# Kernel optimization log

Hardware: AMD Instinct MI355X
Metric: run time of the kernel (lower is better)

## Reference

```python
import jax, jax.numpy as jnp
import numpy as np

EPS = 1e-6

def fexp(x, p):
    # signed power used in superquadric parametrization
    return jnp.sign(x) * (jnp.abs(x) + EPS) ** p

def quat_to_rot(q):
    q = q / (jnp.linalg.norm(q, axis=-1, keepdims=True) + EPS)
    w, x, y, z = q[..., 0], q[..., 1], q[..., 2], q[..., 3]
    R = jnp.stack([
        jnp.stack([1 - 2 * (y * y + z * z), 2 * (x * y - w * z), 2 * (x * z + w * y)], -1),
        jnp.stack([2 * (x * y + w * z), 1 - 2 * (x * x + z * z), 2 * (y * z - w * x)], -1),
        jnp.stack([2 * (x * z - w * y), 2 * (y * z + w * x), 1 - 2 * (x * x + y * y)], -1),
    ], -2)
    return R  # (..., 3, 3)

def setup_inputs() -> dict:
    key = jax.random.key(0)
    ks = jax.random.split(key, 9)
    B, M, S, N = 8, 16, 100, 2048
    pcl = jax.random.normal(ks[0], (B, N, 3), jnp.float32)
    translations = 0.5 * jax.random.normal(ks[1], (B, M, 3), jnp.float32)
    rotations = jax.random.normal(ks[2], (B, M, 4), jnp.float32)
    size = 0.2 + 0.6 * jax.random.uniform(ks[3], (B, M, 3), jnp.float32)
    shape_eps = 0.4 + 1.2 * jax.random.uniform(ks[4], (B, M, 2), jnp.float32)
    deformations = 0.6 * jax.random.uniform(ks[5], (B, M, 2), jnp.float32) - 0.3
    probabilities = jax.random.uniform(ks[6], (B, M), jnp.float32, 0.05, 0.95)
    etas = jax.random.uniform(ks[7], (S,), jnp.float32, -np.pi / 2, np.pi / 2)
    omegas = jax.random.uniform(ks[8], (S,), jnp.float32, -np.pi, np.pi)
    return {"pcl": pcl, "translations": translations, "rotations": rotations,
            "size": size, "shape_eps": shape_eps, "deformations": deformations,
            "probabilities": probabilities, "etas": etas, "omegas": omegas}

def reference(pcl, translations, rotations, size, shape_eps, deformations, probabilities, etas, omegas):
    B, N, _ = pcl.shape
    M = translations.shape[1]
    # transform pcl into primitive-centric frames: (B,N,M,3)
    R = quat_to_rot(rotations)                                   # (B,M,3,3)
    d = pcl[:, :, None, :] - translations[:, None, :, :]         # (B,N,M,3)
    pcl_t = jnp.einsum('bmij,bnmj->bnmi', R, d)                  # (B,N,M,3)
    # sample superquadric surfaces: (B,M,S,3)
    e1 = shape_eps[..., 0:1]; e2 = shape_eps[..., 1:2]           # (B,M,1)
    a1 = size[..., 0:1]; a2 = size[..., 1:2]; a3 = size[..., 2:3]
    ce = fexp(jnp.cos(etas)[None, None, :], e1)
    se = fexp(jnp.sin(etas)[None, None, :], e1)
    cw = fexp(jnp.cos(omegas)[None, None, :], e2)
    sw = fexp(jnp.sin(omegas)[None, None, :], e2)
    x = a1 * ce * cw; y = a2 * ce * sw; z = a3 * se              # (B,M,S)
    # tapering deformation
    fx = deformations[..., 0:1] * z / a3 + 1.0
    fy = deformations[..., 1:2] * z / a3 + 1.0
    points = jnp.stack([fx * x, fy * y, z], -1)                  # (B,M,S,3)
    # pairwise squared distances: (B,M,S,N)
    diff = points[:, :, :, None, :] - jnp.transpose(pcl_t, (0, 2, 1, 3))[:, :, None, :, :]
    dist = jnp.sum(diff * diff, -1)
    # --- pcl_to_prim loss ---
    dmin = jnp.transpose(jnp.min(dist, axis=2), (0, 2, 1))       # (B,N,M)
    idx = jnp.argsort(dmin, axis=-1)
    distance = jnp.take_along_axis(dmin, idx, axis=-1)
    probs_g = jax.vmap(lambda p, i: p[i])(probabilities, idx)    # (B,N,M)
    neg_cp = jnp.cumprod(1.0 - probs_g, axis=-1)
    neg_cp = jnp.concatenate([jnp.ones_like(neg_cp[..., :1]), neg_cp[..., :-1]], -1)
    minprob = probs_g * neg_cp
    pcl_to_prim = jnp.sum(distance * minprob) / (B * N)
    # --- prim_to_pcl loss ---
    dminN = jnp.min(dist, axis=3)                                # (B,M,S)
    dminN = jnp.where(dminN >= 1e30, 0.0, dminN)
    s0, s1, s2 = size[..., 0], size[..., 1], size[..., 2]
    area = 4 * np.pi * ((s0 * s1) ** 1.6 / 3 + (s0 * s2) ** 1.6 / 3 + (s1 * s2) ** 1.6 / 3) ** 0.625
    area = M * area / jnp.sum(area, axis=-1, keepdims=True)
    prim_to_pcl = jnp.sum(jnp.mean(dminN, -1) * area) / (B * M)
    # regularizer weights are zero (regularizer_type=None path) -> regs = 0
    return pcl_to_prim + prim_to_pcl
```

## Files before the change

### kernel.cpp

```cpp
#include <hip/hip_runtime.h>
#include <math.h>

#define EPSF 1e-6f

constexpr int B = 8, N = 2048, M = 16, S = 100;
constexpr int MAIN_BLOCKS = B * (N / 64);
constexpr int PRIM_BLOCKS = B * M * 2;
constexpr int TOTAL_BLOCKS = MAIN_BLOCKS + PRIM_BLOCKS;
constexpr int NPART = MAIN_BLOCKS * 4 + PRIM_BLOCKS;

typedef float v2f __attribute__((ext_vector_type(2)));

__device__ __forceinline__ float hw_exp2(float x) { return __builtin_amdgcn_exp2f(x); }
__device__ __forceinline__ float hw_log2(float x) { return __builtin_amdgcn_logf(x); }

__device__ __forceinline__ float fexp_d(float x, float p) {
    float sg = (x > 0.f) ? 1.f : ((x < 0.f) ? -1.f : 0.f);
    return sg * __powf(fabsf(x) + EPSF, p);
}

__device__ __forceinline__ float sgn_d(float x) {
    return (x > 0.f) ? 1.f : ((x < 0.f) ? -1.f : 0.f);
}

__device__ __forceinline__ void quat_Rv(float w, float x, float y, float z, float R[9]) {
    float inv = 1.0f / (sqrtf(w * w + x * x + y * y + z * z) + EPSF);
    w *= inv; x *= inv; y *= inv; z *= inv;
    R[0] = 1.f - 2.f * (y * y + z * z); R[1] = 2.f * (x * y - w * z); R[2] = 2.f * (x * z + w * y);
    R[3] = 2.f * (x * y + w * z); R[4] = 1.f - 2.f * (x * x + z * z); R[5] = 2.f * (y * z - w * x);
    R[6] = 2.f * (x * z - w * y); R[7] = 2.f * (y * z + w * x); R[8] = 1.f - 2.f * (x * x + y * y);
}

__device__ __forceinline__ void quat_R(const float* __restrict__ rot, int bm, float R[9]) {
    quat_Rv(rot[bm * 4 + 0], rot[bm * 4 + 1], rot[bm * 4 + 2], rot[bm * 4 + 3], R);
}

__device__ __forceinline__ float4 surf_point(
    const float* __restrict__ sizep, const float* __restrict__ seps,
    const float* __restrict__ deform, const float* __restrict__ etas,
    const float* __restrict__ omegas, int bm, int s)
{
    float e1 = seps[bm * 2 + 0], e2 = seps[bm * 2 + 1];
    float a1 = sizep[bm * 3 + 0], a2 = sizep[bm * 3 + 1], a3 = sizep[bm * 3 + 2];
    float d0 = deform[bm * 2 + 0], d1 = deform[bm * 2 + 1];
    float se_, ce_, sw_, cw_;
    __sincosf(etas[s], &se_, &ce_);
    __sincosf(omegas[s], &sw_, &cw_);
    float ce = fexp_d(ce_, e1);
    float se = fexp_d(se_, e1);
    float cw = fexp_d(cw_, e2);
    float sw = fexp_d(sw_, e2);
    float x = a1 * ce * cw;
    float y = a2 * ce * sw;
    float z = a3 * se;
    float fx = d0 * (z / a3) + 1.0f;
    float fy = d1 * (z / a3) + 1.0f;
    float4 P;
    P.x = fx * x; P.y = fy * y; P.z = z;
    P.w = P.x * P.x + P.y * P.y + P.z * P.z;
    return P;
}

__global__ __launch_bounds__(256) void k_all(
    const float* __restrict__ pcl, const float* __restrict__ trans,
    const float* __restrict__ rot, const float* __restrict__ sizep,
    const float* __restrict__ seps, const float* __restrict__ deform,
    const float* __restrict__ probs,
    const float* __restrict__ etas, const float* __restrict__ omegas,
    float* __restrict__ part, unsigned int* __restrict__ flags,
    float* __restrict__ out)
{
    __shared__ float4 pts[S * M];
    __shared__ __align__(16) float trig[S * 8];
    __shared__ float sbuf[20];

    int t = threadIdx.x;

    if (blockIdx.x < MAIN_BLOCKS) {
        int b  = blockIdx.x >> 5;
        int n0 = (blockIdx.x & 31) * 64;
        int m  = t & 15;
        int nl = t >> 4;
        int bm = b * M + m;

        float qw = rot[bm * 4 + 0], qx = rot[bm * 4 + 1];
        float qy = rot[bm * 4 + 2], qz = rot[bm * 4 + 3];
        float tx = trans[bm * 3 + 0], ty = trans[bm * 3 + 1], tz = trans[bm * 3 + 2];
        float plx[4], ply[4], plz[4];
#pragma unroll
        for (int j = 0; j < 4; j++) {
            int n = n0 + nl + 16 * j;
            plx[j] = pcl[(b * N + n) * 3 + 0];
            ply[j] = pcl[(b * N + n) * 3 + 1];
            plz[j] = pcl[(b * N + n) * 3 + 2];
        }
        float pv = probs[bm];

        float4* trig4 = (float4*)trig;
        if (t < S) {
            float se_, ce_, sw_, cw_;
            __sincosf(etas[t], &se_, &ce_);
            __sincosf(omegas[t], &sw_, &cw_);
            float4 tA, tB;
            tA.x = hw_log2(fabsf(ce_) + EPSF); tA.y = sgn_d(ce_);
            tA.z = hw_log2(fabsf(se_) + EPSF); tA.w = sgn_d(se_);
            tB.x = hw_log2(fabsf(cw_) + EPSF); tB.y = sgn_d(cw_);
            tB.z = hw_log2(fabsf(sw_) + EPSF); tB.w = sgn_d(sw_);
            trig4[t * 2 + 0] = tA;
            trig4[t * 2 + 1] = tB;
        }
        __syncthreads();

        {
            float e1 = seps[bm * 2 + 0], e2 = seps[bm * 2 + 1];
            float a1 = sizep[bm * 3 + 0], a2 = sizep[bm * 3 + 1], a3 = sizep[bm * 3 + 2];
            float d0 = deform[bm * 2 + 0], d1 = deform[bm * 2 + 1];
            for (int s = nl; s < S; s += 16) {
                float4 tA = trig4[s * 2 + 0];
                float4 tB = trig4[s * 2 + 1];
                float ce = tA.y * hw_exp2(e1 * tA.x);
                float se = tA.w * hw_exp2(e1 * tA.z);
                float cw = tB.y * hw_exp2(e2 * tB.x);
                float sw = tB.w * hw_exp2(e2 * tB.z);
                float x = a1 * ce * cw;
                float y = a2 * ce * sw;
                float z = a3 * se;
                float fx = fmaf(d0, se, 1.0f);
                float fy = fmaf(d1, se, 1.0f);
                float4 P;
                P.x = fx * x; P.y = fy * y; P.z = z;
                P.w = P.x * P.x + P.y * P.y + P.z * P.z;
                pts[s * M + m] = P;
            }
        }
        __syncthreads();

        float R[9];
        quat_Rv(qw, qx, qy, qz, R);

        v2f mx2[2], my2[2], mz2[2], dmin2[2];
        float psq[4];
#pragma unroll
        for (int j = 0; j < 4; j++) {
            float dx = plx[j] - tx, dy = ply[j] - ty, dz = plz[j] - tz;
            float X = R[0] * dx + R[1] * dy + R[2] * dz;
            float Y = R[3] * dx + R[4] * dy + R[5] * dz;
            float Z = R[6] * dx + R[7] * dy + R[8] * dz;
            mx2[j >> 1][j & 1] = -2.f * X;
            my2[j >> 1][j & 1] = -2.f * Y;
            mz2[j >> 1][j & 1] = -2.f * Z;
            psq[j] = X * X + Y * Y + Z * Z;
            dmin2[j >> 1][j & 1] = 3.4e38f;
        }

        auto compute4 = [&](const float4* P4) {
#pragma unroll
            for (int u = 0; u < 4; u++) {
                float4 P = P4[u];
                v2f vx = {P.x, P.x}, vy = {P.y, P.y}, vz = {P.z, P.z}, vw = {P.w, P.w};
#pragma unroll
                for (int p = 0; p < 2; p++) {
                    v2f d = __builtin_elementwise_fma(vx, mx2[p], vw);
                    d = __builtin_elementwise_fma(vy, my2[p], d);
                    d = __builtin_elementwise_fma(vz, mz2[p], d);
                    dmin2[p] = __builtin_elementwise_min(dmin2[p], d);
                }
            }
        };
        auto load8 = [&](float4* dst, int sbase) {
#pragma unroll
            for (int u = 0; u < 8; u++) dst[u] = pts[(sbase + u) * M + m];
        };

        float4 Abank[8], Bbank[8];
        load8(Abank, 0);
        for (int gp = 0; gp < 6; gp++) {
            load8(Bbank, (2 * gp + 1) * 8);
            compute4(Abank); compute4(Abank + 4);
            if (gp < 5) load8(Abank, (2 * gp + 2) * 8);
            else {
#pragma unroll
                for (int u = 0; u < 4; u++) Abank[u] = pts[(96 + u) * M + m];
            }
            compute4(Bbank); compute4(Bbank + 4);
        }
        compute4(Abank);

        float ompr[16];
#pragma unroll
        for (int k = 0; k < 16; k++) ompr[k] = 1.f - probs[b * M + k];
        float acc = 0.f;
#pragma unroll
        for (int j = 0; j < 4; j++) {
            float key = dmin2[j >> 1][j & 1] + psq[j];
            float prod = 1.f;
#pragma unroll
            for (int k = 0; k < 16; k++) {
                float bk = __shfl(key, k, 16);
                bool before = (bk < key) || (bk == key && k < m);
                prod *= before ? ompr[k] : 1.f;
            }
            acc += key * pv * prod;
        }
        for (int off = 32; off >= 1; off >>= 1) acc += __shfl_down(acc, off);
        if ((t & 63) == 0)
            __hip_atomic_store(&part[blockIdx.x * 4 + (t >> 6)],
                               acc * (1.0f / (B * N)),
                               __ATOMIC_RELAXED, __HIP_MEMORY_SCOPE_AGENT);
        __syncthreads();
        if (t == 0)
            __hip_atomic_store(&flags[blockIdx.x], 1u,
                               __ATOMIC_RELEASE, __HIP_MEMORY_SCOPE_AGENT);
    } else {
        int pb = blockIdx.x - MAIN_BLOCKS;
        int bm = pb >> 1, q = pb & 1;
        int b = bm >> 4, m = bm & 15;
        int s0 = q * 50;

        float4* spts = pts;
        float* sarea = sbuf;
        float* wsum  = sbuf + 16;

        if (t < 50) spts[t] = surf_point(sizep, seps, deform, etas, omegas, bm, s0 + t);
        if (t >= 64 && t < 64 + M) {
            int mm = t - 64;
            float s0s = sizep[(b * M + mm) * 3 + 0];
            float s1s = sizep[(b * M + mm) * 3 + 1];
            float s2s = sizep[(b * M + mm) * 3 + 2];
            float tt = __powf(s0s * s1s, 1.6f) / 3.f + __powf(s0s * s2s, 1.6f) / 3.f
                     + __powf(s1s * s2s, 1.6f) / 3.f;
            sarea[mm] = 4.0f * 3.14159265358979323846f * __powf(tt, 0.625f);
        }
        __syncthreads();

        float R[9];
        quat_R(rot, bm, R);
        float tx = trans[bm * 3 + 0], ty = trans[bm * 3 + 1], tz = trans[bm * 3 + 2];

        int w = t >> 6, lane = t & 63;
        int cnt = (w < 2) ? 13 : 12;
        int off = (w < 2) ? w * 13 : 26 + (w - 2) * 12;

        v2f px2[7], py2[7], pz2[7], mins2[7];
#pragma unroll
        for (int k = 0; k < 14; k++) {
            int sl = (k < cnt) ? (off + k) : off;
            float4 P = spts[sl];
            px2[k >> 1][k & 1] = P.x;
            py2[k >> 1][k & 1] = P.y;
            pz2[k >> 1][k & 1] = P.z;
            mins2[k >> 1][k & 1] = 3.4e38f;
        }

        const float* pcb = pcl + b * N * 3 + lane * 3;

#define LOADG(x0,y0,z0,x1,y1,z1,x2,y2,z2,x3,y3,z3, g)            \
        { const float* p_ = pcb + (g) * 768;                     \
          x0 = p_[0];   y0 = p_[1];   z0 = p_[2];                \
          x1 = p_[192]; y1 = p_[193]; z1 = p_[194];              \
          x2 = p_[384]; y2 = p_[385]; z2 = p_[386];              \
          x3 = p_[576]; y3 = p_[577]; z3 = p_[578]; }

#define COMP1(cx,cy,cz)                                          \
        { float dx = (cx) - tx, dy = (cy) - ty, dz = (cz) - tz;  \
          float X = R[0] * dx + R[1] * dy + R[2] * dz;           \
          float Y = R[3] * dx + R[4] * dy + R[5] * dz;           \
          float Z = R[6] * dx + R[7] * dy + R[8] * dz;           \
          float Xsq = X * X + Y * Y + Z * Z;                     \
          v2f vmX = {-2.f * X, -2.f * X}, vmY = {-2.f * Y, -2.f * Y}; \
          v2f vmZ = {-2.f * Z, -2.f * Z}, vXq = {Xsq, Xsq};      \
          _Pragma("unroll")                                      \
          for (int k = 0; k < 7; k++) {                          \
              v2f d = __builtin_elementwise_fma(px2[k], vmX, vXq); \
              d = __builtin_elementwise_fma(py2[k], vmY, d);     \
              d = __builtin_elementwise_fma(pz2[k], vmZ, d);     \
              mins2[k] = __builtin_elementwise_min(mins2[k], d); \
          } }

#define COMPG(x0,y0,z0,x1,y1,z1,x2,y2,z2,x3,y3,z3)               \
        COMP1(x0,y0,z0) COMP1(x1,y1,z1) COMP1(x2,y2,z2) COMP1(x3,y3,z3)

        float a0x,a0y,a0z,a1x,a1y,a1z,a2x,a2y,a2z,a3x,a3y,a3z;
        float b0x,b0y,b0z,b1x,b1y,b1z,b2x,b2y,b2z,b3x,b3y,b3z;

        LOADG(a0x,a0y,a0z,a1x,a1y,a1z,a2x,a2y,a2z,a3x,a3y,a3z, 0)
        LOADG(b0x,b0y,b0z,b1x,b1y,b1z,b2x,b2y,b2z,b3x,b3y,b3z, 1)
        COMPG(a0x,a0y,a0z,a1x,a1y,a1z,a2x,a2y,a2z,a3x,a3y,a3z)
        LOADG(a0x,a0y,a0z,a1x,a1y,a1z,a2x,a2y,a2z,a3x,a3y,a3z, 2)
        COMPG(b0x,b0y,b0z,b1x,b1y,b1z,b2x,b2y,b2z,b3x,b3y,b3z)
        LOADG(b0x,b0y,b0z,b1x,b1y,b1z,b2x,b2y,b2z,b3x,b3y,b3z, 3)
        COMPG(a0x,a0y,a0z,a1x,a1y,a1z,a2x,a2y,a2z,a3x,a3y,a3z)
        LOADG(a0x,a0y,a0z,a1x,a1y,a1z,a2x,a2y,a2z,a3x,a3y,a3z, 4)
        COMPG(b0x,b0y,b0z,b1x,b1y,b1z,b2x,b2y,b2z,b3x,b3y,b3z)
        LOADG(b0x,b0y,b0z,b1x,b1y,b1z,b2x,b2y,b2z,b3x,b3y,b3z, 5)
        COMPG(a0x,a0y,a0z,a1x,a1y,a1z,a2x,a2y,a2z,a3x,a3y,a3z)
        LOADG(a0x,a0y,a0z,a1x,a1y,a1z,a2x,a2y,a2z,a3x,a3y,a3z, 6)
        COMPG(b0x,b0y,b0z,b1x,b1y,b1z,b2x,b2y,b2z,b3x,b3y,b3z)
        LOADG(b0x,b0y,b0z,b1x,b1y,b1z,b2x,b2y,b2z,b3x,b3y,b3z, 7)
        COMPG(a0x,a0y,a0z,a1x,a1y,a1z,a2x,a2y,a2z,a3x,a3y,a3z)
        COMPG(b0x,b0y,b0z,b1x,b1y,b1z,b2x,b2y,b2z,b3x,b3y,b3z)

#undef LOADG
#undef COMP1
#undef COMPG

        float sum = 0.f;
#pragma unroll
        for (int k = 0; k < 14; k++) {
            float v = mins2[k >> 1][k & 1];
            for (int o = 32; o >= 1; o >>= 1) v = fminf(v, __shfl_down(v, o));
            int sl = (k < cnt) ? (off + k) : off;
            v += spts[sl].w;
            sum += (k < cnt) ? v : 0.f;
        }

        if (lane == 0) wsum[w] = sum;
        __syncthreads();
        if (t == 0) {
            float total = wsum[0] + wsum[1] + wsum[2] + wsum[3];
            float asum = 0.f;
            for (int mm = 0; mm < M; mm++) asum += sarea[mm];
            float area = (float)M * sarea[m] / asum;
            __hip_atomic_store(&part[MAIN_BLOCKS * 4 + pb],
                               total * area * (1.0f / (S * B * M)),
                               __ATOMIC_RELAXED, __HIP_MEMORY_SCOPE_AGENT);
            __hip_atomic_store(&flags[blockIdx.x], 1u,
                               __ATOMIC_RELEASE, __HIP_MEMORY_SCOPE_AGENT);
        }

        if (blockIdx.x == TOTAL_BLOCKS - 1 && t < 64) {
            for (int i = t; i < TOTAL_BLOCKS; i += 64) {
                while (__hip_atomic_load(&flags[i], __ATOMIC_ACQUIRE,
                                         __HIP_MEMORY_SCOPE_AGENT) != 1u)
                    __builtin_amdgcn_s_sleep(2);
            }
            __threadfence();
            float ssum = 0.f;
            for (int i = t; i < NPART; i += 64)
                ssum += __hip_atomic_load(&part[i], __ATOMIC_RELAXED,
                                          __HIP_MEMORY_SCOPE_AGENT);
            for (int off = 32; off >= 1; off >>= 1) ssum += __shfl_down(ssum, off);
            if (t == 0) out[0] = ssum;
            for (int i = t; i < TOTAL_BLOCKS; i += 64)
                __hip_atomic_store(&flags[i], 0u, __ATOMIC_RELAXED,
                                   __HIP_MEMORY_SCOPE_AGENT);
        }
    }
}

extern "C" void kernel_launch(void* const* d_in, const int* in_sizes, int n_in,
                              void* d_out, int out_size, void* d_ws, size_t ws_size,
                              hipStream_t stream)
{
    const float* pcl    = (const float*)d_in[0];
    const float* trans  = (const float*)d_in[1];
    const float* rot    = (const float*)d_in[2];
    const float* sizep  = (const float*)d_in[3];
    const float* seps   = (const float*)d_in[4];
    const float* deform = (const float*)d_in[5];
    const float* probs  = (const float*)d_in[6];
    const float* etas   = (const float*)d_in[7];
    const float* omegas = (const float*)d_in[8];
    float* out = (float*)d_out;
    float* partials = (float*)d_ws;
    unsigned int* flags = (unsigned int*)((char*)d_ws + 8192);

    k_all<<<TOTAL_BLOCKS, 256, 0, stream>>>(pcl, trans, rot, sizep, seps,
                                            deform, probs, etas, omegas,
                                            partials, flags, out);
}
```

Measured before the change: 88.25 us.

## Precompute superquadric surface points in a separate staging kernel

Moves generation of the sampled surface points out of every main block into a small pre-kernel with one block per batch, which writes them to workspace memory. The main blocks then copy the precomputed points from global memory into shared memory instead of recomputing trig, log and exp per block. This removes redundant transcendental work and one barrier per block. In exchange it adds a second kernel launch, a dependency between the two kernels, and global-memory traffic for the points.

```diff
diff --git a/kernel.cpp b/kernel.cpp
--- a/kernel.cpp
+++ b/kernel.cpp
@@ -13,11 +13,6 @@
 
 __device__ __forceinline__ float hw_exp2(float x) { return __builtin_amdgcn_exp2f(x); }
 __device__ __forceinline__ float hw_log2(float x) { return __builtin_amdgcn_logf(x); }
-
-__device__ __forceinline__ float fexp_d(float x, float p) {
-    float sg = (x > 0.f) ? 1.f : ((x < 0.f) ? -1.f : 0.f);
-    return sg * __powf(fabsf(x) + EPSF, p);
-}
 
 __device__ __forceinline__ float sgn_d(float x) {
     return (x > 0.f) ? 1.f : ((x < 0.f) ? -1.f : 0.f);
@@ -35,43 +30,62 @@
     quat_Rv(rot[bm * 4 + 0], rot[bm * 4 + 1], rot[bm * 4 + 2], rot[bm * 4 + 3], R);
 }
 
-__device__ __forceinline__ float4 surf_point(
+__global__ __launch_bounds__(256) void k_stage(
     const float* __restrict__ sizep, const float* __restrict__ seps,
     const float* __restrict__ deform, const float* __restrict__ etas,
-    const float* __restrict__ omegas, int bm, int s)
+    const float* __restrict__ omegas, float4* __restrict__ gpts)
 {
-    float e1 = seps[bm * 2 + 0], e2 = seps[bm * 2 + 1];
-    float a1 = sizep[bm * 3 + 0], a2 = sizep[bm * 3 + 1], a3 = sizep[bm * 3 + 2];
-    float d0 = deform[bm * 2 + 0], d1 = deform[bm * 2 + 1];
-    float se_, ce_, sw_, cw_;
-    __sincosf(etas[s], &se_, &ce_);
-    __sincosf(omegas[s], &sw_, &cw_);
-    float ce = fexp_d(ce_, e1);
-    float se = fexp_d(se_, e1);
-    float cw = fexp_d(cw_, e2);
-    float sw = fexp_d(sw_, e2);
-    float x = a1 * ce * cw;
-    float y = a2 * ce * sw;
-    float z = a3 * se;
-    float fx = d0 * (z / a3) + 1.0f;
-    float fy = d1 * (z / a3) + 1.0f;
-    float4 P;
-    P.x = fx * x; P.y = fy * y; P.z = z;
-    P.w = P.x * P.x + P.y * P.y + P.z * P.z;
-    return P;
+    __shared__ __align__(16) float trig[S * 8];
+    int t = threadIdx.x;
+    int b = blockIdx.x;
+    float4* trig4 = (float4*)trig;
+
+    if (t < S) {
+        float se_, ce_, sw_, cw_;
+        __sincosf(etas[t], &se_, &ce_);
+        __sincosf(omegas[t], &sw_, &cw_);
+        float4 tA, tB;
+        tA.x = hw_log2(fabsf(ce_) + EPSF); tA.y = sgn_d(ce_);
+        tA.z = hw_log2(fabsf(se_) + EPSF); tA.w = sgn_d(se_);
+        tB.x = hw_log2(fabsf(cw_) + EPSF); tB.y = sgn_d(cw_);
+        tB.z = hw_log2(fabsf(sw_) + EPSF); tB.w = sgn_d(sw_);
+        trig4[t * 2 + 0] = tA;
+        trig4[t * 2 + 1] = tB;
+    }
+    __syncthreads();
+
+    int m  = t & 15;
+    int bmi = b * M + m;
+    float e1 = seps[bmi * 2 + 0], e2 = seps[bmi * 2 + 1];
+    float a1 = sizep[bmi * 3 + 0], a2 = sizep[bmi * 3 + 1], a3 = sizep[bmi * 3 + 2];
+    float d0 = deform[bmi * 2 + 0], d1 = deform[bmi * 2 + 1];
+    for (int s = t >> 4; s < S; s += 16) {
+        float4 tA = trig4[s * 2 + 0];
+        float4 tB = trig4[s * 2 + 1];
+        float ce = tA.y * hw_exp2(e1 * tA.x);
+        float se = tA.w * hw_exp2(e1 * tA.z);
+        float cw = tB.y * hw_exp2(e2 * tB.x);
+        float sw = tB.w * hw_exp2(e2 * tB.z);
+        float x = a1 * ce * cw;
+        float y = a2 * ce * sw;
+        float z = a3 * se;
+        float fx = fmaf(d0, se, 1.0f);
+        float fy = fmaf(d1, se, 1.0f);
+        float4 P;
+        P.x = fx * x; P.y = fy * y; P.z = z;
+        P.w = P.x * P.x + P.y * P.y + P.z * P.z;
+        gpts[b * (S * M) + s * M + m] = P;
+    }
 }
 
 __global__ __launch_bounds__(256) void k_all(
     const float* __restrict__ pcl, const float* __restrict__ trans,
     const float* __restrict__ rot, const float* __restrict__ sizep,
-    const float* __restrict__ seps, const float* __restrict__ deform,
-    const float* __restrict__ probs,
-    const float* __restrict__ etas, const float* __restrict__ omegas,
+    const float* __restrict__ probs, const float4* __restrict__ gpts,
     float* __restrict__ part, unsigned int* __restrict__ flags,
     float* __restrict__ out)
 {
     __shared__ float4 pts[S * M];
-    __shared__ __align__(16) float trig[S * 8];
     __shared__ float sbuf[20];
 
     int t = threadIdx.x;
@@ -96,42 +110,9 @@
         }
         float pv = probs[bm];
 
-        float4* trig4 = (float4*)trig;
-        if (t < S) {
-            float se_, ce_, sw_, cw_;
-            __sincosf(etas[t], &se_, &ce_);
-            __sincosf(omegas[t], &sw_, &cw_);
-            float4 tA, tB;
-            tA.x = hw_log2(fabsf(ce_) + EPSF); tA.y = sgn_d(ce_);
-            tA.z = hw_log2(fabsf(se_) + EPSF); tA.w = sgn_d(se_);
-            tB.x = hw_log2(fabsf(cw_) + EPSF); tB.y = sgn_d(cw_);
-            tB.z = hw_log2(fabsf(sw_) + EPSF); tB.w = sgn_d(sw_);
-            trig4[t * 2 + 0] = tA;
-            trig4[t * 2 + 1] = tB;
-        }
-        __syncthreads();
-
         {
-            float e1 = seps[bm * 2 + 0], e2 = seps[bm * 2 + 1];
-            float a1 = sizep[bm * 3 + 0], a2 = sizep[bm * 3 + 1], a3 = sizep[bm * 3 + 2];
-            float d0 = deform[bm * 2 + 0], d1 = deform[bm * 2 + 1];
-            for (int s = nl; s < S; s += 16) {
-                float4 tA = trig4[s * 2 + 0];
-                float4 tB = trig4[s * 2 + 1];
-                float ce = tA.y * hw_exp2(e1 * tA.x);
-                float se = tA.w * hw_exp2(e1 * tA.z);
-                float cw = tB.y * hw_exp2(e2 * tB.x);
-                float sw = tB.w * hw_exp2(e2 * tB.z);
-                float x = a1 * ce * cw;
-                float y = a2 * ce * sw;
-                float z = a3 * se;
-                float fx = fmaf(d0, se, 1.0f);
-                float fy = fmaf(d1, se, 1.0f);
-                float4 P;
-                P.x = fx * x; P.y = fy * y; P.z = z;
-                P.w = P.x * P.x + P.y * P.y + P.z * P.z;
-                pts[s * M + m] = P;
-            }
+            const float4* src = gpts + b * (S * M);
+            for (int i = t; i < S * M; i += 256) pts[i] = src[i];
         }
         __syncthreads();
 
@@ -221,7 +202,7 @@
         float* sarea = sbuf;
         float* wsum  = sbuf + 16;
 
-        if (t < 50) spts[t] = surf_point(sizep, seps, deform, etas, omegas, bm, s0 + t);
+        if (t < 50) spts[t] = gpts[b * (S * M) + (s0 + t) * M + m];
         if (t >= 64 && t < 64 + M) {
             int mm = t - 64;
             float s0s = sizep[(b * M + mm) * 3 + 0];
@@ -364,8 +345,9 @@
     float* out = (float*)d_out;
     float* partials = (float*)d_ws;
     unsigned int* flags = (unsigned int*)((char*)d_ws + 8192);
-
-    k_all<<<TOTAL_BLOCKS, 256, 0, stream>>>(pcl, trans, rot, sizep, seps,
-                                            deform, probs, etas, omegas,
+    float4* gpts = (float4*)((char*)d_ws + 16384);
+
+    k_stage<<<B, 256, 0, stream>>>(sizep, seps, deform, etas, omegas, gpts);
+    k_all<<<TOTAL_BLOCKS, 256, 0, stream>>>(pcl, trans, rot, sizep, probs, gpts,
                                             partials, flags, out);
 }
```

Result: slower. 90.90 us (+3.0%).
